# Performance work log

Hardware: AMD Instinct MI355X
Metric: run time of the kernel (lower is better)

The kernel has to match this reference:

```python
import jax, jax.numpy as jnp
import numpy as np

B = 2048   # number of samples; acts as seq_len for the (S,N,E) transformer
DIN = 768
D = 512    # hidden_dim
H = 8      # nheads
HD = D // H
L = 3      # encoder layers
P = 40     # num_prototypes
Q = D // 4 # 128, projected feature dim
EPS = 1e-5


def setup_inputs() -> dict:
    key = jax.random.key(0)
    ks = jax.random.split(key, 22)
    s = 0.02
    rn = lambda k, shape: jax.random.normal(k, shape, jnp.float32) * s
    return {
        "x": jax.random.normal(ks[0], (B, DIN), jnp.float32),
        "reduce_w": rn(ks[1], (D, DIN)), "reduce_b": rn(ks[2], (D,)),
        "in_w": rn(ks[3], (L, 3 * D, D)), "in_b": rn(ks[4], (L, 3 * D)),
        "out_w": rn(ks[5], (L, D, D)), "out_b": rn(ks[6], (L, D)),
        "ff1_w": rn(ks[7], (L, D, D)), "ff1_b": rn(ks[8], (L, D)),
        "ff2_w": rn(ks[9], (L, D, D)), "ff2_b": rn(ks[10], (L, D)),
        "ln1_w": jnp.ones((L, D), jnp.float32), "ln1_b": jnp.zeros((L, D), jnp.float32),
        "ln2_w": jnp.ones((L, D), jnp.float32), "ln2_b": jnp.zeros((L, D), jnp.float32),
        "mlp_w1": rn(ks[11], (D, D)), "mlp_b1": rn(ks[12], (D,)),
        "mlp_w2": rn(ks[13], (D, D)), "mlp_b2": rn(ks[14], (D,)),
        "mlp_w3": rn(ks[15], (Q, D)), "mlp_b3": rn(ks[16], (Q,)),
        "highlights": jax.random.normal(ks[17], (P, Q), jnp.float32),
        "negatives": jax.random.normal(ks[18], (P, Q), jnp.float32),
    }


def _inorm(x):
    # InstanceNorm1d (affine=False) on a 2D tensor: per-row normalize over last dim
    m = x.mean(-1, keepdims=True)
    v = ((x - m) ** 2).mean(-1, keepdims=True)  # biased variance, matches torch
    return (x - m) * jax.lax.rsqrt(v + EPS)


def _ln(x, w, b):
    m = x.mean(-1, keepdims=True)
    v = ((x - m) ** 2).mean(-1, keepdims=True)
    return (x - m) * jax.lax.rsqrt(v + EPS) * w + b


def _cdist(a, cb):
    # euclidean distances [B,P]
    d2 = (a * a).sum(-1, keepdims=True) + (cb * cb).sum(-1) - 2.0 * a @ cb.T
    return jnp.sqrt(jnp.maximum(d2, 0.0))


def reference(x, reduce_w, reduce_b, in_w, in_b, out_w, out_b,
              ff1_w, ff1_b, ff2_w, ff2_b, ln1_w, ln1_b, ln2_w, ln2_b,
              mlp_w1, mlp_b1, mlp_w2, mlp_b2, mlp_w3, mlp_b3,
              highlights, negatives):
    feat0 = _inorm(x @ reduce_w.T + reduce_b)  # [B,D]

    # TransformerEncoder, post-norm, relu FFN, dropout off (eval).
    # Input is (seq=B, batch=1, D) -> attention across all B rows.
    feat = feat0
    scale = 1.0 / np.sqrt(HD)
    for i in range(L):
        qkv = feat @ in_w[i].T + in_b[i]           # [B,3D]
        q, k, v = jnp.split(qkv, 3, axis=-1)
        q = q.reshape(B, H, HD)
        k = k.reshape(B, H, HD)
        v = v.reshape(B, H, HD)
        scores = jnp.einsum('ihd,jhd->hij', q, k) * scale  # [H,B,B]
        attn = jax.nn.softmax(scores, axis=-1)
        ctx = jnp.einsum('hij,jhd->ihd', attn, v).reshape(B, D)
        attn_out = ctx @ out_w[i].T + out_b[i]
        feat = _ln(feat + attn_out, ln1_w[i], ln1_b[i])
        ff = jax.nn.relu(feat @ ff1_w[i].T + ff1_b[i]) @ ff2_w[i].T + ff2_b[i]
        feat = _ln(feat + ff, ln2_w[i], ln2_b[i])

    feat = feat0 + _inorm(feat)

    # MLP 512 -> 512 -> 512 -> 128 (relu on all but last)
    feat = jax.nn.relu(feat @ mlp_w1.T + mlp_b1)
    feat = jax.nn.relu(feat @ mlp_w2.T + mlp_b2)
    feat = feat @ mlp_w3.T + mlp_b3
    feat = _inorm(feat)  # [B,Q]

    positive_dist = _cdist(feat, highlights).min(-1)
    negative_dist = _cdist(feat, negatives).min(-1)
    logits = jnp.stack([-negative_dist, -positive_dist], axis=-1)  # [B,2]
    return logits
```

## Files before the change

### kernel.cpp

```cpp
#include <hip/hip_runtime.h>
#include <math.h>
#include <cstddef>

#define EPS 1e-5f

typedef __attribute__((ext_vector_type(8))) short bf16x8;
typedef __attribute__((ext_vector_type(4))) float f32x4;

__device__ __forceinline__ float wave_sum(float v) {
#pragma unroll
  for (int o = 32; o > 0; o >>= 1) v += __shfl_xor(v, o, 64);
  return v;
}

__device__ __forceinline__ unsigned short f2b(float f) {
  union { float f; unsigned int u; } v; v.f = f;
  unsigned int r = (v.u + 0x7FFFu + ((v.u >> 16) & 1u)) >> 16;
  return (unsigned short)r;
}
__device__ __forceinline__ float b2f(unsigned short u) {
  union { unsigned int u; float f; } v; v.u = ((unsigned int)u) << 16;
  return v.f;
}

__device__ __forceinline__ unsigned int pk2(float lo, float hi) {
  unsigned int r;
  asm volatile("v_cvt_pk_bf16_f32 %0, %1, %2" : "=v"(r) : "v"(lo), "v"(hi));
  return r;
}

struct WConvArgs {
  const float* src[8];
  unsigned short* dst[8];
  int n[8];
};
__global__ __launch_bounds__(256) void conv_w(WConvArgs a) {
  const int arr = blockIdx.y;
  const int i = (blockIdx.x * 256 + threadIdx.x) * 4;
  if (i >= a.n[arr]) return;
  const float4 f = *(const float4*)(a.src[arr] + i);
  unsigned short t[4] = {f2b(f.x), f2b(f.y), f2b(f.z), f2b(f.w)};
  unsigned short* d = a.dst[arr] + i;
  *(ushort2*)d = *(ushort2*)&t[0];
  *(ushort2*)(d + 2) = *(ushort2*)&t[2];
}

template <int RELU, int AF32, int OUT_F32, int OUT_BF16, int MERGE, int RESID,
          int SCALEQ>
__global__ __launch_bounds__(256) void gemm32(
    const void* __restrict__ Aptr, const float* __restrict__ pmp,
    const unsigned short* __restrict__ W, const float* __restrict__ bias,
    const float* __restrict__ Rf, float* __restrict__ Cf,
    unsigned short* __restrict__ Cb, int M, int N, int K) {
  __shared__ __align__(16) unsigned short As[2][32][72];
  __shared__ __align__(16) unsigned short Ws[2][64][72];
  const int tid = threadIdx.x;
  const int wid = tid >> 6, lane = tid & 63;
  const int ln = lane & 15, quad = lane >> 4;
  const int m0 = blockIdx.x * 32, n0 = blockIdx.y * 64;
  const int arow = tid >> 3, aseg = tid & 7;
  const int wrow = tid >> 2, wseg = tid & 3;
  const int KS = K >> 6;

  bf16x8 ra;
  float4 ra32[2];
  bf16x8 rwb0, rwb1;
  bf16x8 rp[4];
  float rl;

  auto load_tile = [&](int ks) {
    const int k0 = ks * 64;
    if (MERGE) {
      const int h = ks;
      const int row = m0 + arow;
      rl = 0.f;
#pragma unroll
      for (int s = 0; s < 4; ++s) {
        const size_t b = (size_t)((s * 8 + h) * 2048 + row);
        rl += pmp[b];
        rp[s] = *(const bf16x8*)((const unsigned short*)Aptr + b * 64 + aseg * 8);
      }
    } else if (AF32) {
      const float* ap = (const float*)Aptr + (size_t)(m0 + arow) * K + k0 + aseg * 8;
      ra32[0] = *(const float4*)ap;
      ra32[1] = *(const float4*)(ap + 4);
    } else {
      ra = *(const bf16x8*)((const unsigned short*)Aptr +
                            (size_t)(m0 + arow) * K + k0 + aseg * 8);
    }
    const unsigned short* wp = W + (size_t)(n0 + wrow) * K + k0 + wseg * 16;
    rwb0 = *(const bf16x8*)wp;
    rwb1 = *(const bf16x8*)(wp + 8);
  };

  auto store_tile = [&](int buf) {
    if (MERGE) {
      float inv = 1.f / rl;
      unsigned short ta[8];
#pragma unroll
      for (int j = 0; j < 8; ++j) {
        float s = b2f((unsigned short)rp[0][j]) + b2f((unsigned short)rp[1][j]) +
                  b2f((unsigned short)rp[2][j]) + b2f((unsigned short)rp[3][j]);
        ta[j] = f2b(inv * s);
      }
      *(bf16x8*)&As[buf][arow][aseg * 8] = *(const bf16x8*)&ta[0];
    } else if (AF32) {
      unsigned short ta[8];
      ta[0] = f2b(ra32[0].x); ta[1] = f2b(ra32[0].y);
      ta[2] = f2b(ra32[0].z); ta[3] = f2b(ra32[0].w);
      ta[4] = f2b(ra32[1].x); ta[5] = f2b(ra32[1].y);
      ta[6] = f2b(ra32[1].z); ta[7] = f2b(ra32[1].w);
      *(bf16x8*)&As[buf][arow][aseg * 8] = *(const bf16x8*)&ta[0];
    } else {
      *(bf16x8*)&As[buf][arow][aseg * 8] = ra;
    }
    *(bf16x8*)&Ws[buf][wrow][wseg * 16] = rwb0;
    *(bf16x8*)&Ws[buf][wrow][wseg * 16 + 8] = rwb1;
  };

  f32x4 acc[2];
  acc[0] = (f32x4){0.f, 0.f, 0.f, 0.f};
  acc[1] = (f32x4){0.f, 0.f, 0.f, 0.f};

  const int mrow = (wid & 1) * 16, nh = wid >> 1;

  load_tile(0);
  store_tile(0);
  __syncthreads();

#pragma unroll 1
  for (int ks = 0; ks < KS; ++ks) {
    const int cur = ks & 1;
    if (ks + 1 < KS) load_tile(ks + 1);
#pragma unroll
    for (int kc = 0; kc < 2; ++kc) {
      bf16x8 af = *(const bf16x8*)&As[cur][mrow + ln][kc * 32 + quad * 8];
#pragma unroll
      for (int nt = 0; nt < 2; ++nt) {
        bf16x8 wf = *(const bf16x8*)&Ws[cur][nh * 32 + nt * 16 + ln][kc * 32 + quad * 8];
        acc[nt] = __builtin_amdgcn_mfma_f32_16x16x32_bf16(af, wf, acc[nt], 0, 0, 0);
      }
    }
    if (ks + 1 < KS) store_tile(cur ^ 1);
    __syncthreads();
  }

  const int gm = m0 + mrow + quad * 4;
  const float qs = (SCALEQ && n0 < 512) ? 0.125f : 1.f;
#pragma unroll
  for (int nt = 0; nt < 2; ++nt) {
    const int gn = n0 + nh * 32 + nt * 16 + ln;
    float bv = bias[gn];
#pragma unroll
    for (int r = 0; r < 4; ++r) {
      float v = acc[nt][r] + bv;
      if (SCALEQ) v *= qs;
      if (RELU) v = fmaxf(v, 0.f);
      if (RESID) v += Rf[(size_t)(gm + r) * N + gn];
      if (OUT_F32) Cf[(size_t)(gm + r) * N + gn] = v;
      if (OUT_BF16) Cb[(size_t)(gm + r) * N + gn] = f2b(v);
    }
  }
}

__global__ __launch_bounds__(256) void flash_attn8(
    const unsigned short* __restrict__ qkv, float* __restrict__ pm,
    unsigned short* __restrict__ po) {
  __shared__ __align__(16) unsigned short Ks[64][72];
  __shared__ __align__(16) unsigned short Vt[64][72];
  __shared__ __align__(16) unsigned int Pp[64][36];
  const int qt = blockIdx.x, h = blockIdx.y, sp = blockIdx.z;
  const int tid = threadIdx.x;
  const int wid = tid >> 6, lane = tid & 63;
  const int ln = lane & 15, quad = lane >> 4;
  const int wq0 = wid * 16;

  bf16x8 aq[2];
  {
    const unsigned short* qp =
        qkv + (size_t)(qt * 64 + wq0 + ln) * 1536 + h * 64 + quad * 8;
    aq[0] = *(const bf16x8*)qp;
    aq[1] = *(const bf16x8*)(qp + 32);
  }

  const int key = tid >> 2, seg = tid & 3;
  bf16x8 rk0, rk1;
  unsigned short tv[16];

  auto load_kv = [&](int t) {
    const int g = sp * 8 + t;
    const unsigned short* kr =
        qkv + (size_t)(g * 64 + key) * 1536 + 512 + h * 64 + seg * 16;
    rk0 = *(const bf16x8*)kr;
    rk1 = *(const bf16x8*)(kr + 8);
#pragma unroll
    for (int j = 0; j < 16; ++j)
      tv[j] = qkv[(size_t)(g * 64 + wid * 16 + j) * 1536 + 1024 + h * 64 + lane];
  };
  auto store_kv = [&]() {
    *(bf16x8*)&Ks[key][seg * 16] = rk0;
    *(bf16x8*)&Ks[key][seg * 16 + 8] = rk1;
    *(bf16x8*)&Vt[lane][wid * 16] = *(const bf16x8*)&tv[0];
    *(bf16x8*)&Vt[lane][wid * 16 + 8] = *(const bf16x8*)&tv[8];
  };

  float l_r = 0.f;
  f32x4 acc_o[4];
#pragma unroll
  for (int nt = 0; nt < 4; ++nt) acc_o[nt] = (f32x4){0.f, 0.f, 0.f, 0.f};

  load_kv(0);
  store_kv();
  __syncthreads();

#pragma unroll 1
  for (int t = 0; t < 8; ++t) {
    if (t + 1 < 8) load_kv(t + 1);

    f32x4 s_acc[4];
#pragma unroll
    for (int nt = 0; nt < 4; ++nt) s_acc[nt] = (f32x4){0.f, 0.f, 0.f, 0.f};
#pragma unroll
    for (int nt = 0; nt < 4; ++nt) {
      bf16x8 kf0 = *(const bf16x8*)&Ks[nt * 16 + ln][quad * 8];
      bf16x8 kf1 = *(const bf16x8*)&Ks[nt * 16 + ln][32 + quad * 8];
      s_acc[nt] = __builtin_amdgcn_mfma_f32_16x16x32_bf16(kf0, aq[0], s_acc[nt], 0, 0, 0);
      s_acc[nt] = __builtin_amdgcn_mfma_f32_16x16x32_bf16(kf1, aq[1], s_acc[nt], 0, 0, 0);
    }

#pragma unroll
    for (int nt = 0; nt < 4; ++nt) {
      float p0 = __expf(s_acc[nt][0]);
      float p1 = __expf(s_acc[nt][1]);
      float p2 = __expf(s_acc[nt][2]);
      float p3 = __expf(s_acc[nt][3]);
      l_r += (p0 + p1) + (p2 + p3);
      uint2 w;
      w.x = pk2(p0, p1);
      w.y = pk2(p2, p3);
      *(uint2*)&Pp[wq0 + ln][nt * 8 + quad * 2] = w;
    }

#pragma unroll
    for (int kc = 0; kc < 2; ++kc) {
      bf16x8 pf = *(const bf16x8*)&Pp[wq0 + ln][kc * 16 + quad * 4];
#pragma unroll
      for (int nt = 0; nt < 4; ++nt) {
        bf16x8 vf = *(const bf16x8*)&Vt[nt * 16 + ln][kc * 32 + quad * 8];
        acc_o[nt] = __builtin_amdgcn_mfma_f32_16x16x32_bf16(pf, vf, acc_o[nt], 0, 0, 0);
      }
    }
    __syncthreads();
    if (t + 1 < 8) {
      store_kv();
      __syncthreads();
    }
  }

  const size_t base = (size_t)((sp * 8 + h) * 2048 + qt * 64);
  float l = l_r;
  l += __shfl_xor(l, 16, 64);
  l += __shfl_xor(l, 32, 64);
  if (quad == 0) pm[base + wq0 + ln] = l;
#pragma unroll
  for (int r = 0; r < 4; ++r) {
    const size_t row = base + wq0 + quad * 4 + r;
#pragma unroll
    for (int nt = 0; nt < 4; ++nt)
      po[row * 64 + nt * 16 + ln] = f2b(acc_o[nt][r]);
  }
}

__global__ __launch_bounds__(256) void inorm512(float* __restrict__ dst,
                                                unsigned short* __restrict__ dstb,
                                                const float* __restrict__ src) {
  const int row = blockIdx.x * 4 + (threadIdx.x >> 6);
  const int lane = threadIdx.x & 63;
  const float4* s = (const float4*)(src + (size_t)row * 512);
  float4 a = s[lane], b = s[lane + 64];
  float sum = a.x + a.y + a.z + a.w + b.x + b.y + b.z + b.w;
  float mean = wave_sum(sum) * (1.f / 512.f);
  float vs = (a.x - mean) * (a.x - mean) + (a.y - mean) * (a.y - mean) +
             (a.z - mean) * (a.z - mean) + (a.w - mean) * (a.w - mean) +
             (b.x - mean) * (b.x - mean) + (b.y - mean) * (b.y - mean) +
             (b.z - mean) * (b.z - mean) + (b.w - mean) * (b.w - mean);
  float rs = rsqrtf(wave_sum(vs) * (1.f / 512.f) + EPS);
  float4 oa, obv;
  oa.x = (a.x - mean) * rs; oa.y = (a.y - mean) * rs;
  oa.z = (a.z - mean) * rs; oa.w = (a.w - mean) * rs;
  obv.x = (b.x - mean) * rs; obv.y = (b.y - mean) * rs;
  obv.z = (b.z - mean) * rs; obv.w = (b.w - mean) * rs;
  float4* d = (float4*)(dst + (size_t)row * 512);
  d[lane] = oa; d[lane + 64] = obv;
  unsigned short* db = dstb + (size_t)row * 512;
  unsigned short t0[4] = {f2b(oa.x), f2b(oa.y), f2b(oa.z), f2b(oa.w)};
  unsigned short t1[4] = {f2b(obv.x), f2b(obv.y), f2b(obv.z), f2b(obv.w)};
  *(ushort2*)&db[lane * 4] = *(ushort2*)&t0[0];
  *(ushort2*)&db[lane * 4 + 2] = *(ushort2*)&t0[2];
  *(ushort2*)&db[256 + lane * 4] = *(ushort2*)&t1[0];
  *(ushort2*)&db[256 + lane * 4 + 2] = *(ushort2*)&t1[2];
}

__global__ __launch_bounds__(256) void ln_res2(float* __restrict__ dst,
                                               unsigned short* __restrict__ dstb,
                                               const float* __restrict__ src,
                                               const float* __restrict__ w,
                                               const float* __restrict__ bb) {
  const int row = blockIdx.x * 4 + (threadIdx.x >> 6);
  const int lane = threadIdx.x & 63;
  const float4* xs = (const float4*)(src + (size_t)row * 512);
  float4 a = xs[lane], b = xs[lane + 64];
  float sum = a.x + a.y + a.z + a.w + b.x + b.y + b.z + b.w;
  float mean = wave_sum(sum) * (1.f / 512.f);
  float vs = (a.x - mean) * (a.x - mean) + (a.y - mean) * (a.y - mean) +
             (a.z - mean) * (a.z - mean) + (a.w - mean) * (a.w - mean) +
             (b.x - mean) * (b.x - mean) + (b.y - mean) * (b.y - mean) +
             (b.z - mean) * (b.z - mean) + (b.w - mean) * (b.w - mean);
  float rs = rsqrtf(wave_sum(vs) * (1.f / 512.f) + EPS);
  float4 wa = ((const float4*)w)[lane], wb = ((const float4*)w)[lane + 64];
  float4 ba = ((const float4*)bb)[lane], bbv = ((const float4*)bb)[lane + 64];
  float4 oa, ob2;
  oa.x = (a.x - mean) * rs * wa.x + ba.x; oa.y = (a.y - mean) * rs * wa.y + ba.y;
  oa.z = (a.z - mean) * rs * wa.z + ba.z; oa.w = (a.w - mean) * rs * wa.w + ba.w;
  ob2.x = (b.x - mean) * rs * wb.x + bbv.x; ob2.y = (b.y - mean) * rs * wb.y + bbv.y;
  ob2.z = (b.z - mean) * rs * wb.z + bbv.z; ob2.w = (b.w - mean) * rs * wb.w + bbv.w;
  float4* d = (float4*)(dst + (size_t)row * 512);
  d[lane] = oa; d[lane + 64] = ob2;
  unsigned short* dbp = dstb + (size_t)row * 512;
  unsigned short t0[4] = {f2b(oa.x), f2b(oa.y), f2b(oa.z), f2b(oa.w)};
  unsigned short t1[4] = {f2b(ob2.x), f2b(ob2.y), f2b(ob2.z), f2b(ob2.w)};
  *(ushort2*)&dbp[lane * 4] = *(ushort2*)&t0[0];
  *(ushort2*)&dbp[lane * 4 + 2] = *(ushort2*)&t0[2];
  *(ushort2*)&dbp[256 + lane * 4] = *(ushort2*)&t1[0];
  *(ushort2*)&dbp[256 + lane * 4 + 2] = *(ushort2*)&t1[2];
}

__global__ __launch_bounds__(256) void add_inorm(float* __restrict__ feat,
                                                 unsigned short* __restrict__ featb,
                                                 const float* __restrict__ feat0) {
  const int row = blockIdx.x * 4 + (threadIdx.x >> 6);
  const int lane = threadIdx.x & 63;
  float4* f = (float4*)(feat + (size_t)row * 512);
  const float4* f0 = (const float4*)(feat0 + (size_t)row * 512);
  float4 a = f[lane], b = f[lane + 64];
  float sum = a.x + a.y + a.z + a.w + b.x + b.y + b.z + b.w;
  float mean = wave_sum(sum) * (1.f / 512.f);
  float vs = (a.x - mean) * (a.x - mean) + (a.y - mean) * (a.y - mean) +
             (a.z - mean) * (a.z - mean) + (a.w - mean) * (a.w - mean) +
             (b.x - mean) * (b.x - mean) + (b.y - mean) * (b.y - mean) +
             (b.z - mean) * (b.z - mean) + (b.w - mean) * (b.w - mean);
  float rs = rsqrtf(wave_sum(vs) * (1.f / 512.f) + EPS);
  float4 za = f0[lane], zb = f0[lane + 64];
  float4 oa, ob2;
  oa.x = za.x + (a.x - mean) * rs; oa.y = za.y + (a.y - mean) * rs;
  oa.z = za.z + (a.z - mean) * rs; oa.w = za.w + (a.w - mean) * rs;
  ob2.x = zb.x + (b.x - mean) * rs; ob2.y = zb.y + (b.y - mean) * rs;
  ob2.z = zb.z + (b.z - mean) * rs; ob2.w = zb.w + (b.w - mean) * rs;
  f[lane] = oa; f[lane + 64] = ob2;
  unsigned short* dbp = featb + (size_t)row * 512;
  unsigned short t0[4] = {f2b(oa.x), f2b(oa.y), f2b(oa.z), f2b(oa.w)};
  unsigned short t1[4] = {f2b(ob2.x), f2b(ob2.y), f2b(ob2.z), f2b(ob2.w)};
  *(ushort2*)&dbp[lane * 4] = *(ushort2*)&t0[0];
  *(ushort2*)&dbp[lane * 4 + 2] = *(ushort2*)&t0[2];
  *(ushort2*)&dbp[256 + lane * 4] = *(ushort2*)&t1[0];
  *(ushort2*)&dbp[256 + lane * 4 + 2] = *(ushort2*)&t1[2];
}

__global__ __launch_bounds__(256) void dist2(const float* __restrict__ fq,
                                             const float* __restrict__ hi,
                                             const float* __restrict__ ne,
                                             float* __restrict__ out) {
  const int row = blockIdx.x * 4 + (threadIdx.x >> 6);
  const int lane = threadIdx.x & 63;
  float f0 = fq[(size_t)row * 128 + lane];
  float f1 = fq[(size_t)row * 128 + 64 + lane];
  float mean = wave_sum(f0 + f1) * (1.f / 128.f);
  float vs = (f0 - mean) * (f0 - mean) + (f1 - mean) * (f1 - mean);
  float rs = rsqrtf(wave_sum(vs) * (1.f / 128.f) + EPS);
  f0 = (f0 - mean) * rs;
  f1 = (f1 - mean) * rs;
  float mp = 1e30f, mn = 1e30f;
  for (int p = 0; p < 40; ++p) {
    float h0 = hi[p * 128 + lane], h1 = hi[p * 128 + 64 + lane];
    float d0 = f0 - h0, d1 = f1 - h1;
    float d2 = wave_sum(d0 * d0 + d1 * d1);
    mp = fminf(mp, d2);
    float n0 = ne[p * 128 + lane], n1 = ne[p * 128 + 64 + lane];
    d0 = f0 - n0; d1 = f1 - n1;
    d2 = wave_sum(d0 * d0 + d1 * d1);
    mn = fminf(mn, d2);
  }
  if (lane == 0) {
    out[row * 2 + 0] = -sqrtf(mn);
    out[row * 2 + 1] = -sqrtf(mp);
  }
}

extern "C" void kernel_launch(void* const* d_in, const int* in_sizes, int n_in,
                              void* d_out, int out_size, void* d_ws, size_t ws_size,
                              hipStream_t stream) {
  const float* x        = (const float*)d_in[0];
  const float* reduce_w = (const float*)d_in[1];
  const float* reduce_b = (const float*)d_in[2];
  const float* in_w     = (const float*)d_in[3];
  const float* in_b     = (const float*)d_in[4];
  const float* out_w    = (const float*)d_in[5];
  const float* out_b    = (const float*)d_in[6];
  const float* ff1_w    = (const float*)d_in[7];
  const float* ff1_b    = (const float*)d_in[8];
  const float* ff2_w    = (const float*)d_in[9];
  const float* ff2_b    = (const float*)d_in[10];
  const float* ln1_w    = (const float*)d_in[11];
  const float* ln1_b    = (const float*)d_in[12];
  const float* ln2_w    = (const float*)d_in[13];
  const float* ln2_b    = (const float*)d_in[14];
  const float* mlp_w1   = (const float*)d_in[15];
  const float* mlp_b1   = (const float*)d_in[16];
  const float* mlp_w2   = (const float*)d_in[17];
  const float* mlp_b2   = (const float*)d_in[18];
  const float* mlp_w3   = (const float*)d_in[19];
  const float* mlp_b3   = (const float*)d_in[20];
  const float* hi       = (const float*)d_in[21];
  const float* ne       = (const float*)d_in[22];
  float* out = (float*)d_out;
  float* ws = (float*)d_ws;

  const size_t MD = (size_t)2048 * 512;
  float* feat0_f = ws;
  float* feat_f  = ws + MD;
  float* tmp_f   = ws + 2 * MD;
  float* pm      = ws + 3 * MD;
  unsigned short* u = (unsigned short*)(ws + 3 * MD + 65536);
  unsigned short* qkv_b   = u;
  unsigned short* feat0_b = u + 3 * MD;
  unsigned short* feat_b  = u + 4 * MD;
  unsigned short* relu_b  = u + 5 * MD;
  unsigned short* po_b    = u + 6 * MD;
  unsigned short* relu2_b = qkv_b;
  float* featq_f = tmp_f;

  unsigned short* wb = u + 10 * MD;
  unsigned short* reduce_wb = wb;
  unsigned short* in_wb     = wb + 393216;
  unsigned short* out_wb    = in_wb + 2359296;
  unsigned short* ff1_wb    = out_wb + 786432;
  unsigned short* ff2_wb    = ff1_wb + 786432;
  unsigned short* mlp_w1b   = ff2_wb + 786432;
  unsigned short* mlp_w2b   = mlp_w1b + 262144;
  unsigned short* mlp_w3b   = mlp_w2b + 262144;

  dim3 blk(256);
  WConvArgs wa;
  wa.src[0] = reduce_w; wa.dst[0] = reduce_wb; wa.n[0] = 393216;
  wa.src[1] = in_w;     wa.dst[1] = in_wb;     wa.n[1] = 2359296;
  wa.src[2] = out_w;    wa.dst[2] = out_wb;    wa.n[2] = 786432;
  wa.src[3] = ff1_w;    wa.dst[3] = ff1_wb;    wa.n[3] = 786432;
  wa.src[4] = ff2_w;    wa.dst[4] = ff2_wb;    wa.n[4] = 786432;
  wa.src[5] = mlp_w1;   wa.dst[5] = mlp_w1b;   wa.n[5] = 262144;
  wa.src[6] = mlp_w2;   wa.dst[6] = mlp_w2b;   wa.n[6] = 262144;
  wa.src[7] = mlp_w3;   wa.dst[7] = mlp_w3b;   wa.n[7] = 65536;
  conv_w<<<dim3(2304, 8), blk, 0, stream>>>(wa);

  gemm32<0, 1, 1, 0, 0, 0, 0><<<dim3(64, 8), blk, 0, stream>>>(
      x, nullptr, reduce_wb, reduce_b, nullptr, feat0_f, nullptr, 2048, 512, 768);
  inorm512<<<512, blk, 0, stream>>>(feat0_f, feat0_b, feat0_f);

  for (int i = 0; i < 3; ++i) {
    const float* fin_f = (i == 0) ? feat0_f : feat_f;
    const unsigned short* fin_b = (i == 0) ? feat0_b : feat_b;
    gemm32<0, 0, 0, 1, 0, 0, 1><<<dim3(64, 24), blk, 0, stream>>>(
        fin_b, nullptr, in_wb + (size_t)i * 1536 * 512, in_b + i * 1536,
        nullptr, nullptr, qkv_b, 2048, 1536, 512);
    flash_attn8<<<dim3(32, 8, 4), blk, 0, stream>>>(qkv_b, pm, po_b);
    gemm32<0, 0, 1, 0, 1, 1, 0><<<dim3(64, 8), blk, 0, stream>>>(
        po_b, pm, out_wb + (size_t)i * 512 * 512, out_b + i * 512,
        fin_f, tmp_f, nullptr, 2048, 512, 512);
    ln_res2<<<512, blk, 0, stream>>>(feat_f, feat_b, tmp_f,
                                     ln1_w + i * 512, ln1_b + i * 512);
    gemm32<1, 0, 0, 1, 0, 0, 0><<<dim3(64, 8), blk, 0, stream>>>(
        feat_b, nullptr, ff1_wb + (size_t)i * 512 * 512, ff1_b + i * 512,
        nullptr, nullptr, relu_b, 2048, 512, 512);
    gemm32<0, 0, 1, 0, 0, 1, 0><<<dim3(64, 8), blk, 0, stream>>>(
        relu_b, nullptr, ff2_wb + (size_t)i * 512 * 512, ff2_b + i * 512,
        feat_f, tmp_f, nullptr, 2048, 512, 512);
    ln_res2<<<512, blk, 0, stream>>>(feat_f, feat_b, tmp_f,
                                     ln2_w + i * 512, ln2_b + i * 512);
  }

  add_inorm<<<512, blk, 0, stream>>>(feat_f, feat_b, feat0_f);
  gemm32<1, 0, 0, 1, 0, 0, 0><<<dim3(64, 8), blk, 0, stream>>>(
      feat_b, nullptr, mlp_w1b, mlp_b1, nullptr, nullptr, relu_b, 2048, 512, 512);
  gemm32<1, 0, 0, 1, 0, 0, 0><<<dim3(64, 8), blk, 0, stream>>>(
      relu_b, nullptr, mlp_w2b, mlp_b2, nullptr, nullptr, relu2_b, 2048, 512, 512);
  gemm32<0, 0, 1, 0, 0, 0, 0><<<dim3(64, 2), blk, 0, stream>>>(
      relu2_b, nullptr, mlp_w3b, mlp_b3, nullptr, featq_f, nullptr, 2048, 128, 512);
  dist2<<<512, blk, 0, stream>>>(featq_f, hi, ne, out);
}
```

Before: 362.3 us.

## Fuse normalization prologues into GEMMs and stage full A row-block in LDS

Removes the standalone inorm, layernorm and add_inorm kernels by computing the row normalization inside the prologue of the following GEMM. Each block loads its whole 32xK A tile into shared memory once and streams only the weights, with blockIdx.y==0 writing the fp32 normalized rows for later residual use. This saves several launches and the fp32/bf16 intermediate round trips. In exchange, every N-tile block recomputes the same row statistics (24x for QKV), uses more LDS, and no longer overlaps the A loads with compute.

```diff
diff --git a/kernel.cpp b/kernel.cpp
--- a/kernel.cpp
+++ b/kernel.cpp
@@ -27,6 +27,13 @@
   unsigned int r;
   asm volatile("v_cvt_pk_bf16_f32 %0, %1, %2" : "=v"(r) : "v"(lo), "v"(hi));
   return r;
+}
+
+__device__ __forceinline__ bf16x8 pack8(const float* o) {
+  union { unsigned int u[4]; bf16x8 v; } r;
+  r.u[0] = pk2(o[0], o[1]); r.u[1] = pk2(o[2], o[3]);
+  r.u[2] = pk2(o[4], o[5]); r.u[3] = pk2(o[6], o[7]);
+  return r.v;
 }
 
 struct WConvArgs {
@@ -45,75 +52,128 @@
   *(ushort2*)(d + 2) = *(ushort2*)&t[2];
 }
 
-template <int RELU, int AF32, int OUT_F32, int OUT_BF16, int MERGE, int RESID,
-          int SCALEQ>
-__global__ __launch_bounds__(256) void gemm32(
+template <int RELU, int PRO, int OUT_F32, int OUT_BF16, int RESID, int SCALEQ,
+          int WRB, int KK>
+__global__ __launch_bounds__(256) void gemm2(
     const void* __restrict__ Aptr, const float* __restrict__ pmp,
+    const float* __restrict__ lnw, const float* __restrict__ lnb,
+    const float* __restrict__ add0, float* __restrict__ wrb,
     const unsigned short* __restrict__ W, const float* __restrict__ bias,
     const float* __restrict__ Rf, float* __restrict__ Cf,
-    unsigned short* __restrict__ Cb, int M, int N, int K) {
-  __shared__ __align__(16) unsigned short As[2][32][72];
+    unsigned short* __restrict__ Cb, int N) {
+  __shared__ __align__(16) unsigned short As[32][KK + 8];
   __shared__ __align__(16) unsigned short Ws[2][64][72];
   const int tid = threadIdx.x;
   const int wid = tid >> 6, lane = tid & 63;
   const int ln = lane & 15, quad = lane >> 4;
   const int m0 = blockIdx.x * 32, n0 = blockIdx.y * 64;
-  const int arow = tid >> 3, aseg = tid & 7;
+
+  if (PRO == 0) {
+    const int row = tid >> 3, seg = tid & 7;
+    const unsigned short* ap =
+        (const unsigned short*)Aptr + (size_t)(m0 + row) * KK + seg * 8;
+#pragma unroll
+    for (int j = 0; j < KK / 64; ++j)
+      *(bf16x8*)&As[row][seg * 8 + j * 64] = *(const bf16x8*)(ap + j * 64);
+  } else if (PRO == 1) {
+    const int row = tid >> 3, seg = tid & 7;
+    const float* ap = (const float*)Aptr + (size_t)(m0 + row) * KK + seg * 8;
+#pragma unroll
+    for (int j = 0; j < KK / 64; ++j) {
+      float4 a = *(const float4*)(ap + j * 64);
+      float4 b = *(const float4*)(ap + j * 64 + 4);
+      float o[8] = {a.x, a.y, a.z, a.w, b.x, b.y, b.z, b.w};
+      *(bf16x8*)&As[row][seg * 8 + j * 64] = pack8(o);
+    }
+  } else if (PRO == 5) {
+    const int row = tid >> 3, seg = tid & 7;
+    const unsigned short* pob = (const unsigned short*)Aptr;
+#pragma unroll
+    for (int j = 0; j < 8; ++j) {
+      float l = pmp[(size_t)j * 2048 + m0 + row] +
+                pmp[(size_t)(8 + j) * 2048 + m0 + row] +
+                pmp[(size_t)(16 + j) * 2048 + m0 + row] +
+                pmp[(size_t)(24 + j) * 2048 + m0 + row];
+      float inv = 1.f / l;
+      float o[8] = {0.f, 0.f, 0.f, 0.f, 0.f, 0.f, 0.f, 0.f};
+#pragma unroll
+      for (int s = 0; s < 4; ++s) {
+        bf16x8 v = *(const bf16x8*)(
+            pob + ((size_t)((s * 8 + j) * 2048 + m0 + row)) * 64 + seg * 8);
+#pragma unroll
+        for (int k = 0; k < 8; ++k) o[k] += b2f((unsigned short)v[k]);
+      }
+#pragma unroll
+      for (int k = 0; k < 8; ++k) o[k] *= inv;
+      *(bf16x8*)&As[row][j * 64 + seg * 8] = pack8(o);
+    }
+  } else {
+    float wv[8], bv[8];
+    if (PRO == 3 || PRO == 4) {
+      float4 w0 = *(const float4*)(lnw + lane * 8);
+      float4 w1 = *(const float4*)(lnw + lane * 8 + 4);
+      float4 b0 = *(const float4*)(lnb + lane * 8);
+      float4 b1 = *(const float4*)(lnb + lane * 8 + 4);
+      wv[0] = w0.x; wv[1] = w0.y; wv[2] = w0.z; wv[3] = w0.w;
+      wv[4] = w1.x; wv[5] = w1.y; wv[6] = w1.z; wv[7] = w1.w;
+      bv[0] = b0.x; bv[1] = b0.y; bv[2] = b0.z; bv[3] = b0.w;
+      bv[4] = b1.x; bv[5] = b1.y; bv[6] = b1.z; bv[7] = b1.w;
+    }
+#pragma unroll
+    for (int rr = 0; rr < 8; ++rr) {
+      const int row = wid * 8 + rr;
+      const float* ap = (const float*)Aptr + (size_t)(m0 + row) * 512 + lane * 8;
+      float4 a = *(const float4*)ap, b = *(const float4*)(ap + 4);
+      float o[8] = {a.x, a.y, a.z, a.w, b.x, b.y, b.z, b.w};
+      float s = 0.f, ss = 0.f;
+#pragma unroll
+      for (int k = 0; k < 8; ++k) s += o[k];
+      float mean = wave_sum(s) * (1.f / 512.f);
+#pragma unroll
+      for (int k = 0; k < 8; ++k) { float d = o[k] - mean; ss += d * d; }
+      float rs = rsqrtf(wave_sum(ss) * (1.f / 512.f) + EPS);
+#pragma unroll
+      for (int k = 0; k < 8; ++k) o[k] = (o[k] - mean) * rs;
+      if (PRO == 3 || PRO == 4) {
+#pragma unroll
+        for (int k = 0; k < 8; ++k) o[k] = o[k] * wv[k] + bv[k];
+      }
+      if (PRO == 4) {
+        float s2 = 0.f, ss2 = 0.f;
+#pragma unroll
+        for (int k = 0; k < 8; ++k) s2 += o[k];
+        float m2 = wave_sum(s2) * (1.f / 512.f);
+#pragma unroll
+        for (int k = 0; k < 8; ++k) { float d = o[k] - m2; ss2 += d * d; }
+        float rs2 = rsqrtf(wave_sum(ss2) * (1.f / 512.f) + EPS);
+        const float* zp = add0 + (size_t)(m0 + row) * 512 + lane * 8;
+        float4 z0 = *(const float4*)zp, z1 = *(const float4*)(zp + 4);
+        float z[8] = {z0.x, z0.y, z0.z, z0.w, z1.x, z1.y, z1.z, z1.w};
+#pragma unroll
+        for (int k = 0; k < 8; ++k) o[k] = z[k] + (o[k] - m2) * rs2;
+      }
+      if (WRB) {
+        if (blockIdx.y == 0) {
+          float* dp = wrb + (size_t)(m0 + row) * 512 + lane * 8;
+          float4 o0 = {o[0], o[1], o[2], o[3]};
+          float4 o1 = {o[4], o[5], o[6], o[7]};
+          *(float4*)dp = o0;
+          *(float4*)(dp + 4) = o1;
+        }
+      }
+      *(bf16x8*)&As[row][lane * 8] = pack8(o);
+    }
+  }
+
   const int wrow = tid >> 2, wseg = tid & 3;
-  const int KS = K >> 6;
-
-  bf16x8 ra;
-  float4 ra32[2];
+  const int KS = KK / 64;
   bf16x8 rwb0, rwb1;
-  bf16x8 rp[4];
-  float rl;
-
-  auto load_tile = [&](int ks) {
-    const int k0 = ks * 64;
-    if (MERGE) {
-      const int h = ks;
-      const int row = m0 + arow;
-      rl = 0.f;
-#pragma unroll
-      for (int s = 0; s < 4; ++s) {
-        const size_t b = (size_t)((s * 8 + h) * 2048 + row);
-        rl += pmp[b];
-        rp[s] = *(const bf16x8*)((const unsigned short*)Aptr + b * 64 + aseg * 8);
-      }
-    } else if (AF32) {
-      const float* ap = (const float*)Aptr + (size_t)(m0 + arow) * K + k0 + aseg * 8;
-      ra32[0] = *(const float4*)ap;
-      ra32[1] = *(const float4*)(ap + 4);
-    } else {
-      ra = *(const bf16x8*)((const unsigned short*)Aptr +
-                            (size_t)(m0 + arow) * K + k0 + aseg * 8);
-    }
-    const unsigned short* wp = W + (size_t)(n0 + wrow) * K + k0 + wseg * 16;
+  auto load_w = [&](int ks) {
+    const unsigned short* wp = W + (size_t)(n0 + wrow) * KK + ks * 64 + wseg * 16;
     rwb0 = *(const bf16x8*)wp;
     rwb1 = *(const bf16x8*)(wp + 8);
   };
-
-  auto store_tile = [&](int buf) {
-    if (MERGE) {
-      float inv = 1.f / rl;
-      unsigned short ta[8];
-#pragma unroll
-      for (int j = 0; j < 8; ++j) {
-        float s = b2f((unsigned short)rp[0][j]) + b2f((unsigned short)rp[1][j]) +
-                  b2f((unsigned short)rp[2][j]) + b2f((unsigned short)rp[3][j]);
-        ta[j] = f2b(inv * s);
-      }
-      *(bf16x8*)&As[buf][arow][aseg * 8] = *(const bf16x8*)&ta[0];
-    } else if (AF32) {
-      unsigned short ta[8];
-      ta[0] = f2b(ra32[0].x); ta[1] = f2b(ra32[0].y);
-      ta[2] = f2b(ra32[0].z); ta[3] = f2b(ra32[0].w);
-      ta[4] = f2b(ra32[1].x); ta[5] = f2b(ra32[1].y);
-      ta[6] = f2b(ra32[1].z); ta[7] = f2b(ra32[1].w);
-      *(bf16x8*)&As[buf][arow][aseg * 8] = *(const bf16x8*)&ta[0];
-    } else {
-      *(bf16x8*)&As[buf][arow][aseg * 8] = ra;
-    }
+  auto store_w = [&](int buf) {
     *(bf16x8*)&Ws[buf][wrow][wseg * 16] = rwb0;
     *(bf16x8*)&Ws[buf][wrow][wseg * 16 + 8] = rwb1;
   };
@@ -121,27 +181,26 @@
   f32x4 acc[2];
   acc[0] = (f32x4){0.f, 0.f, 0.f, 0.f};
   acc[1] = (f32x4){0.f, 0.f, 0.f, 0.f};
-
   const int mrow = (wid & 1) * 16, nh = wid >> 1;
 
-  load_tile(0);
-  store_tile(0);
+  load_w(0);
+  store_w(0);
   __syncthreads();
 
 #pragma unroll 1
   for (int ks = 0; ks < KS; ++ks) {
     const int cur = ks & 1;
-    if (ks + 1 < KS) load_tile(ks + 1);
+    if (ks + 1 < KS) load_w(ks + 1);
 #pragma unroll
     for (int kc = 0; kc < 2; ++kc) {
-      bf16x8 af = *(const bf16x8*)&As[cur][mrow + ln][kc * 32 + quad * 8];
+      bf16x8 af = *(const bf16x8*)&As[mrow + ln][ks * 64 + kc * 32 + quad * 8];
 #pragma unroll
       for (int nt = 0; nt < 2; ++nt) {
         bf16x8 wf = *(const bf16x8*)&Ws[cur][nh * 32 + nt * 16 + ln][kc * 32 + quad * 8];
         acc[nt] = __builtin_amdgcn_mfma_f32_16x16x32_bf16(af, wf, acc[nt], 0, 0, 0);
       }
     }
-    if (ks + 1 < KS) store_tile(cur ^ 1);
+    if (ks + 1 < KS) store_w(cur ^ 1);
     __syncthreads();
   }
 
@@ -150,10 +209,10 @@
 #pragma unroll
   for (int nt = 0; nt < 2; ++nt) {
     const int gn = n0 + nh * 32 + nt * 16 + ln;
-    float bv = bias[gn];
+    float bvv = bias[gn];
 #pragma unroll
     for (int r = 0; r < 4; ++r) {
-      float v = acc[nt][r] + bv;
+      float v = acc[nt][r] + bvv;
       if (SCALEQ) v *= qs;
       if (RELU) v = fmaxf(v, 0.f);
       if (RESID) v += Rf[(size_t)(gm + r) * N + gn];
@@ -269,101 +328,6 @@
     for (int nt = 0; nt < 4; ++nt)
       po[row * 64 + nt * 16 + ln] = f2b(acc_o[nt][r]);
   }
-}
-
-__global__ __launch_bounds__(256) void inorm512(float* __restrict__ dst,
-                                                unsigned short* __restrict__ dstb,
-                                                const float* __restrict__ src) {
-  const int row = blockIdx.x * 4 + (threadIdx.x >> 6);
-  const int lane = threadIdx.x & 63;
-  const float4* s = (const float4*)(src + (size_t)row * 512);
-  float4 a = s[lane], b = s[lane + 64];
-  float sum = a.x + a.y + a.z + a.w + b.x + b.y + b.z + b.w;
-  float mean = wave_sum(sum) * (1.f / 512.f);
-  float vs = (a.x - mean) * (a.x - mean) + (a.y - mean) * (a.y - mean) +
-             (a.z - mean) * (a.z - mean) + (a.w - mean) * (a.w - mean) +
-             (b.x - mean) * (b.x - mean) + (b.y - mean) * (b.y - mean) +
-             (b.z - mean) * (b.z - mean) + (b.w - mean) * (b.w - mean);
-  float rs = rsqrtf(wave_sum(vs) * (1.f / 512.f) + EPS);
-  float4 oa, obv;
-  oa.x = (a.x - mean) * rs; oa.y = (a.y - mean) * rs;
-  oa.z = (a.z - mean) * rs; oa.w = (a.w - mean) * rs;
-  obv.x = (b.x - mean) * rs; obv.y = (b.y - mean) * rs;
-  obv.z = (b.z - mean) * rs; obv.w = (b.w - mean) * rs;
-  float4* d = (float4*)(dst + (size_t)row * 512);
-  d[lane] = oa; d[lane + 64] = obv;
-  unsigned short* db = dstb + (size_t)row * 512;
-  unsigned short t0[4] = {f2b(oa.x), f2b(oa.y), f2b(oa.z), f2b(oa.w)};
-  unsigned short t1[4] = {f2b(obv.x), f2b(obv.y), f2b(obv.z), f2b(obv.w)};
-  *(ushort2*)&db[lane * 4] = *(ushort2*)&t0[0];
-  *(ushort2*)&db[lane * 4 + 2] = *(ushort2*)&t0[2];
-  *(ushort2*)&db[256 + lane * 4] = *(ushort2*)&t1[0];
-  *(ushort2*)&db[256 + lane * 4 + 2] = *(ushort2*)&t1[2];
-}
-
-__global__ __launch_bounds__(256) void ln_res2(float* __restrict__ dst,
-                                               unsigned short* __restrict__ dstb,
-                                               const float* __restrict__ src,
-                                               const float* __restrict__ w,
-                                               const float* __restrict__ bb) {
-  const int row = blockIdx.x * 4 + (threadIdx.x >> 6);
-  const int lane = threadIdx.x & 63;
-  const float4* xs = (const float4*)(src + (size_t)row * 512);
-  float4 a = xs[lane], b = xs[lane + 64];
-  float sum = a.x + a.y + a.z + a.w + b.x + b.y + b.z + b.w;
-  float mean = wave_sum(sum) * (1.f / 512.f);
-  float vs = (a.x - mean) * (a.x - mean) + (a.y - mean) * (a.y - mean) +
-             (a.z - mean) * (a.z - mean) + (a.w - mean) * (a.w - mean) +
-             (b.x - mean) * (b.x - mean) + (b.y - mean) * (b.y - mean) +
-             (b.z - mean) * (b.z - mean) + (b.w - mean) * (b.w - mean);
-  float rs = rsqrtf(wave_sum(vs) * (1.f / 512.f) + EPS);
-  float4 wa = ((const float4*)w)[lane], wb = ((const float4*)w)[lane + 64];
-  float4 ba = ((const float4*)bb)[lane], bbv = ((const float4*)bb)[lane + 64];
-  float4 oa, ob2;
-  oa.x = (a.x - mean) * rs * wa.x + ba.x; oa.y = (a.y - mean) * rs * wa.y + ba.y;
-  oa.z = (a.z - mean) * rs * wa.z + ba.z; oa.w = (a.w - mean) * rs * wa.w + ba.w;
-  ob2.x = (b.x - mean) * rs * wb.x + bbv.x; ob2.y = (b.y - mean) * rs * wb.y + bbv.y;
-  ob2.z = (b.z - mean) * rs * wb.z + bbv.z; ob2.w = (b.w - mean) * rs * wb.w + bbv.w;
-  float4* d = (float4*)(dst + (size_t)row * 512);
-  d[lane] = oa; d[lane + 64] = ob2;
-  unsigned short* dbp = dstb + (size_t)row * 512;
-  unsigned short t0[4] = {f2b(oa.x), f2b(oa.y), f2b(oa.z), f2b(oa.w)};
-  unsigned short t1[4] = {f2b(ob2.x), f2b(ob2.y), f2b(ob2.z), f2b(ob2.w)};
-  *(ushort2*)&dbp[lane * 4] = *(ushort2*)&t0[0];
-  *(ushort2*)&dbp[lane * 4 + 2] = *(ushort2*)&t0[2];
-  *(ushort2*)&dbp[256 + lane * 4] = *(ushort2*)&t1[0];
-  *(ushort2*)&dbp[256 + lane * 4 + 2] = *(ushort2*)&t1[2];
-}
-
-__global__ __launch_bounds__(256) void add_inorm(float* __restrict__ feat,
-                                                 unsigned short* __restrict__ featb,
-                                                 const float* __restrict__ feat0) {
-  const int row = blockIdx.x * 4 + (threadIdx.x >> 6);
-  const int lane = threadIdx.x & 63;
-  float4* f = (float4*)(feat + (size_t)row * 512);
-  const float4* f0 = (const float4*)(feat0 + (size_t)row * 512);
-  float4 a = f[lane], b = f[lane + 64];
-  float sum = a.x + a.y + a.z + a.w + b.x + b.y + b.z + b.w;
-  float mean = wave_sum(sum) * (1.f / 512.f);
-  float vs = (a.x - mean) * (a.x - mean) + (a.y - mean) * (a.y - mean) +
-             (a.z - mean) * (a.z - mean) + (a.w - mean) * (a.w - mean) +
-             (b.x - mean) * (b.x - mean) + (b.y - mean) * (b.y - mean) +
-             (b.z - mean) * (b.z - mean) + (b.w - mean) * (b.w - mean);
-  float rs = rsqrtf(wave_sum(vs) * (1.f / 512.f) + EPS);
-  float4 za = f0[lane], zb = f0[lane + 64];
-  float4 oa, ob2;
-  oa.x = za.x + (a.x - mean) * rs; oa.y = za.y + (a.y - mean) * rs;
-  oa.z = za.z + (a.z - mean) * rs; oa.w = za.w + (a.w - mean) * rs;
-  ob2.x = zb.x + (b.x - mean) * rs; ob2.y = zb.y + (b.y - mean) * rs;
-  ob2.z = zb.z + (b.z - mean) * rs; ob2.w = zb.w + (b.w - mean) * rs;
-  f[lane] = oa; f[lane + 64] = ob2;
-  unsigned short* dbp = featb + (size_t)row * 512;
-  unsigned short t0[4] = {f2b(oa.x), f2b(oa.y), f2b(oa.z), f2b(oa.w)};
-  unsigned short t1[4] = {f2b(ob2.x), f2b(ob2.y), f2b(ob2.z), f2b(ob2.w)};
-  *(ushort2*)&dbp[lane * 4] = *(ushort2*)&t0[0];
-  *(ushort2*)&dbp[lane * 4 + 2] = *(ushort2*)&t0[2];
-  *(ushort2*)&dbp[256 + lane * 4] = *(ushort2*)&t1[0];
-  *(ushort2*)&dbp[256 + lane * 4 + 2] = *(ushort2*)&t1[2];
 }
 
 __global__ __launch_bounds__(256) void dist2(const float* __restrict__ fq,
@@ -426,20 +390,19 @@
   float* ws = (float*)d_ws;
 
   const size_t MD = (size_t)2048 * 512;
-  float* feat0_f = ws;
-  float* feat_f  = ws + MD;
-  float* tmp_f   = ws + 2 * MD;
-  float* pm      = ws + 3 * MD;
-  unsigned short* u = (unsigned short*)(ws + 3 * MD + 65536);
+  float* feat0_f  = ws;
+  float* feat0n_f = ws + MD;
+  float* feat_f   = ws + 2 * MD;
+  float* tmp_f    = ws + 3 * MD;
+  float* pm       = ws + 4 * MD;
+  unsigned short* u = (unsigned short*)(ws + 4 * MD + 65536);
   unsigned short* qkv_b   = u;
-  unsigned short* feat0_b = u + 3 * MD;
-  unsigned short* feat_b  = u + 4 * MD;
-  unsigned short* relu_b  = u + 5 * MD;
-  unsigned short* po_b    = u + 6 * MD;
+  unsigned short* relu_b  = u + 3 * MD;
+  unsigned short* po_b    = u + 4 * MD;
   unsigned short* relu2_b = qkv_b;
   float* featq_f = tmp_f;
 
-  unsigned short* wb = u + 10 * MD;
+  unsigned short* wb = u + 8 * MD;
   unsigned short* reduce_wb = wb;
   unsigned short* in_wb     = wb + 393216;
   unsigned short* out_wb    = in_wb + 2359296;
@@ -461,38 +424,45 @@
   wa.src[7] = mlp_w3;   wa.dst[7] = mlp_w3b;   wa.n[7] = 65536;
   conv_w<<<dim3(2304, 8), blk, 0, stream>>>(wa);
 
-  gemm32<0, 1, 1, 0, 0, 0, 0><<<dim3(64, 8), blk, 0, stream>>>(
-      x, nullptr, reduce_wb, reduce_b, nullptr, feat0_f, nullptr, 2048, 512, 768);
-  inorm512<<<512, blk, 0, stream>>>(feat0_f, feat0_b, feat0_f);
+  gemm2<0, 1, 1, 0, 0, 0, 0, 768><<<dim3(64, 8), blk, 0, stream>>>(
+      x, nullptr, nullptr, nullptr, nullptr, nullptr,
+      reduce_wb, reduce_b, nullptr, feat0_f, nullptr, 512);
 
   for (int i = 0; i < 3; ++i) {
-    const float* fin_f = (i == 0) ? feat0_f : feat_f;
-    const unsigned short* fin_b = (i == 0) ? feat0_b : feat_b;
-    gemm32<0, 0, 0, 1, 0, 0, 1><<<dim3(64, 24), blk, 0, stream>>>(
-        fin_b, nullptr, in_wb + (size_t)i * 1536 * 512, in_b + i * 1536,
-        nullptr, nullptr, qkv_b, 2048, 1536, 512);
+    if (i == 0) {
+      gemm2<0, 2, 0, 1, 0, 1, 1, 512><<<dim3(64, 24), blk, 0, stream>>>(
+          feat0_f, nullptr, nullptr, nullptr, nullptr, feat0n_f,
+          in_wb, in_b, nullptr, nullptr, qkv_b, 1536);
+    } else {
+      gemm2<0, 3, 0, 1, 0, 1, 1, 512><<<dim3(64, 24), blk, 0, stream>>>(
+          tmp_f, nullptr, ln2_w + (i - 1) * 512, ln2_b + (i - 1) * 512,
+          nullptr, feat_f, in_wb + (size_t)i * 1536 * 512, in_b + i * 1536,
+          nullptr, nullptr, qkv_b, 1536);
+    }
     flash_attn8<<<dim3(32, 8, 4), blk, 0, stream>>>(qkv_b, pm, po_b);
-    gemm32<0, 0, 1, 0, 1, 1, 0><<<dim3(64, 8), blk, 0, stream>>>(
-        po_b, pm, out_wb + (size_t)i * 512 * 512, out_b + i * 512,
-        fin_f, tmp_f, nullptr, 2048, 512, 512);
-    ln_res2<<<512, blk, 0, stream>>>(feat_f, feat_b, tmp_f,
-                                     ln1_w + i * 512, ln1_b + i * 512);
-    gemm32<1, 0, 0, 1, 0, 0, 0><<<dim3(64, 8), blk, 0, stream>>>(
-        feat_b, nullptr, ff1_wb + (size_t)i * 512 * 512, ff1_b + i * 512,
-        nullptr, nullptr, relu_b, 2048, 512, 512);
-    gemm32<0, 0, 1, 0, 0, 1, 0><<<dim3(64, 8), blk, 0, stream>>>(
-        relu_b, nullptr, ff2_wb + (size_t)i * 512 * 512, ff2_b + i * 512,
-        feat_f, tmp_f, nullptr, 2048, 512, 512);
-    ln_res2<<<512, blk, 0, stream>>>(feat_f, feat_b, tmp_f,
-                                     ln2_w + i * 512, ln2_b + i * 512);
-  }
-
-  add_inorm<<<512, blk, 0, stream>>>(feat_f, feat_b, feat0_f);
-  gemm32<1, 0, 0, 1, 0, 0, 0><<<dim3(64, 8), blk, 0, stream>>>(
-      feat_b, nullptr, mlp_w1b, mlp_b1, nullptr, nullptr, relu_b, 2048, 512, 512);
-  gemm32<1, 0, 0, 1, 0, 0, 0><<<dim3(64, 8), blk, 0, stream>>>(
-      relu_b, nullptr, mlp_w2b, mlp_b2, nullptr, nullptr, relu2_b, 2048, 512, 512);
-  gemm32<0, 0, 1, 0, 0, 0, 0><<<dim3(64, 2), blk, 0, stream>>>(
-      relu2_b, nullptr, mlp_w3b, mlp_b3, nullptr, featq_f, nullptr, 2048, 128, 512);
+    const float* fin_f = (i == 0) ? feat0n_f : feat_f;
+    gemm2<0, 5, 1, 0, 1, 0, 0, 512><<<dim3(64, 8), blk, 0, stream>>>(
+        po_b, pm, nullptr, nullptr, nullptr, nullptr,
+        out_wb + (size_t)i * 512 * 512, out_b + i * 512,
+        fin_f, tmp_f, nullptr, 512);
+    gemm2<1, 3, 0, 1, 0, 0, 1, 512><<<dim3(64, 8), blk, 0, stream>>>(
+        tmp_f, nullptr, ln1_w + i * 512, ln1_b + i * 512, nullptr, feat_f,
+        ff1_wb + (size_t)i * 512 * 512, ff1_b + i * 512,
+        nullptr, nullptr, relu_b, 512);
+    gemm2<0, 0, 1, 0, 1, 0, 0, 512><<<dim3(64, 8), blk, 0, stream>>>(
+        relu_b, nullptr, nullptr, nullptr, nullptr, nullptr,
+        ff2_wb + (size_t)i * 512 * 512, ff2_b + i * 512,
+        feat_f, tmp_f, nullptr, 512);
+  }
+
+  gemm2<1, 4, 0, 1, 0, 0, 0, 512><<<dim3(64, 8), blk, 0, stream>>>(
+      tmp_f, nullptr, ln2_w + 2 * 512, ln2_b + 2 * 512, feat0n_f, nullptr,
+      mlp_w1b, mlp_b1, nullptr, nullptr, relu_b, 512);
+  gemm2<1, 0, 0, 1, 0, 0, 0, 512><<<dim3(64, 8), blk, 0, stream>>>(
+      relu_b, nullptr, nullptr, nullptr, nullptr, nullptr,
+      mlp_w2b, mlp_b2, nullptr, nullptr, relu2_b, 512);
+  gemm2<0, 0, 1, 0, 0, 0, 0, 512><<<dim3(64, 2), blk, 0, stream>>>(
+      relu2_b, nullptr, nullptr, nullptr, nullptr, nullptr,
+      mlp_w3b, mlp_b3, nullptr, featq_f, nullptr, 128);
   dist2<<<512, blk, 0, stream>>>(featq_f, hi, ne, out);
 }
```

Result: slower. 375.5 us (+3.7%).
